# Optimization experiments

Hardware: AMD Instinct MI355X
Metric: run time of the kernel (lower is better)

Reference implementation:

```python
import jax, jax.numpy as jnp
import numpy as np

B, T, D_IN, H, NUM_LAYERS = 64, 512, 512, 500, 2


def _lstm_dir(x, mask, W_ih, W_hh, b, reverse):
    """One unidirectional LSTM over padded batch. x:[B,T,D], mask:[B,T,1] bool.
    AllenNLP AugmentedLstm gate order: input, forget, memory(cell), output."""
    bsz = x.shape[0]
    h_dim = W_hh.shape[1]
    # Precompute all input-side gate projections in one big GEMM: [B,T,4H]
    x_gates = jnp.einsum('btd,gd->btg', x, W_ih) + b

    def step(carry, inp):
        h, c = carry
        gx, m = inp  # gx:[B,4H], m:[B,1]
        gates = gx + h @ W_hh.T
        i, f, g, o = jnp.split(gates, 4, axis=-1)
        i = jax.nn.sigmoid(i)
        f = jax.nn.sigmoid(f)
        g = jnp.tanh(g)
        o = jax.nn.sigmoid(o)
        c_new = f * c + i * g
        h_new = o * jnp.tanh(c_new)
        h = jnp.where(m, h_new, h)
        c = jnp.where(m, c_new, c)
        return (h, c), h * m  # padded positions emit zeros (like pad_packed_sequence)

    init = (jnp.zeros((bsz, h_dim), x.dtype), jnp.zeros((bsz, h_dim), x.dtype))
    xs = (jnp.swapaxes(x_gates, 0, 1), jnp.swapaxes(mask, 0, 1))
    _, ys = jax.lax.scan(step, init, xs, reverse=reverse)
    return jnp.swapaxes(ys, 0, 1)  # [B,T,H]


def _stacked_bilstm(seqs, mask, params):
    x = seqs
    for (Wf_ih, Wf_hh, bf, Wb_ih, Wb_hh, bb) in params:
        fwd = _lstm_dir(x, mask, Wf_ih, Wf_hh, bf, reverse=False)
        bwd = _lstm_dir(x, mask, Wb_ih, Wb_hh, bb, reverse=True)
        x = jnp.concatenate([fwd, bwd], axis=-1)
    return x


def setup_inputs() -> dict:
    key = jax.random.key(0)
    ks = jax.random.split(key, 16)
    seqs = jax.random.normal(ks[0], (B, T, D_IN), dtype=jnp.float32)
    lengths = jnp.clip(jax.random.randint(ks[1], (B,), 0, T + 1), 1, T).astype(jnp.int64)
    inp = {'seqs': seqs, 'lengths': lengths}
    scale = 0.05
    d_in = D_IN
    idx = 2
    for l in range(NUM_LAYERS):
        for d in ('f', 'b'):
            inp[f'W_ih{l}{d}'] = jax.random.normal(ks[idx], (4 * H, d_in), dtype=jnp.float32) * scale; idx += 1
            inp[f'W_hh{l}{d}'] = jax.random.normal(ks[idx], (4 * H, H), dtype=jnp.float32) * scale; idx += 1
            inp[f'b{l}{d}'] = jnp.zeros((4 * H,), dtype=jnp.float32)
        d_in = 2 * H
    return inp


def reference(seqs, lengths, W_ih0f, W_hh0f, b0f, W_ih0b, W_hh0b, b0b,
              W_ih1f, W_hh1f, b1f, W_ih1b, W_hh1b, b1b):
    mask = (jnp.arange(T)[None, :] < lengths[:, None])[..., None]  # [B,T,1] bool
    params = [
        (W_ih0f, W_hh0f, b0f, W_ih0b, W_hh0b, b0b),
        (W_ih1f, W_hh1f, b1f, W_ih1b, W_hh1b, b1b),
    ]
    return _stacked_bilstm(seqs, mask, params)  # [B,T,2H]
```

## Files before the change

kernel.cpp:

```cpp
#include <hip/hip_runtime.h>
#include <cstdint>
#include <cstddef>

#define BB   64
#define TT   512
#define HH   500
#define G4H  2000
#define KPAD 512
#define TCH  64
#define D1P  1024
#define NPAD 2048
#define UPB  16
#define NB2  32
#define WSL2 (32 * 64 * 512)

typedef _Float16 v8h __attribute__((ext_vector_type(8)));
typedef _Float16 v4h __attribute__((ext_vector_type(4)));
typedef float    v4f __attribute__((ext_vector_type(4)));

union F16x8 { unsigned long long u[2]; float4 f4; v8h h; };
union H16B  { _Float16 f; unsigned short u; };

__device__ __forceinline__ float sigm(float x) { return 1.f / (1.f + __expf(-x)); }
__device__ __forceinline__ float tanh_fast(float x) {
    float e = __expf(2.f * x);
    return 1.f - 2.f / (e + 1.f);
}

__device__ __forceinline__ void gload_lds16(const _Float16* src, _Float16* dst) {
    __builtin_amdgcn_global_load_lds(
        (const __attribute__((address_space(1))) void*)src,
        (__attribute__((address_space(3))) void*)dst, 16, 0, 0);
}


__global__ __launch_bounds__(256) void pad_whh16_kernel(
    const float* __restrict__ w0, const float* __restrict__ w1,
    const float* __restrict__ w2, const float* __restrict__ w3,
    _Float16* __restrict__ dst)
{
    int idx = blockIdx.x * 256 + threadIdx.x;
    int k = idx & 511;
    int t = idx >> 9;
    int r = t & 63;  t >>= 6;
    int bi = t & 31;
    int ld = t >> 5;
    int g = r >> 4, j = r & 15;
    int u = bi * UPB + j;
    const float* src = (ld == 0) ? w0 : (ld == 1) ? w1 : (ld == 2) ? w2 : w3;
    float val = (u < HH && k < HH) ? src[(size_t)(g * HH + u) * HH + k] : 0.f;
    dst[idx] = (_Float16)val;
}

__global__ __launch_bounds__(256) void pad_wih16_kernel(
    const float* __restrict__ wf, const float* __restrict__ wb,
    _Float16* __restrict__ dst, int ksrc, int kshift)
{
    int idx = blockIdx.x * 256 + threadIdx.x;
    int kdst = 1 << kshift;
    int k = idx & (kdst - 1);
    int n = (idx >> kshift) & (NPAD - 1);
    int d = idx >> (kshift + 11);
    int bi = n >> 6, r = n & 63, g = r >> 4, j = r & 15;
    int u = bi * UPB + j;
    const float* src = d ? wb : wf;
    float v = (u < HH && k < ksrc) ? src[(size_t)(g * HH + u) * ksrc + k] : 0.f;
    dst[idx] = (_Float16)v;
}

__global__ __launch_bounds__(256) void bias_perm_kernel(
    const float* __restrict__ b0f_, const float* __restrict__ b0b_,
    const float* __restrict__ b1f_, const float* __restrict__ b1b_,
    float* __restrict__ dst)
{
    int idx = blockIdx.x * 256 + threadIdx.x;
    int n = idx & (NPAD - 1);
    int ld = idx >> 11;
    int bi = n >> 6, r = n & 63, g = r >> 4, j = r & 15;
    int u = bi * UPB + j;
    const float* src = (ld == 0) ? b0f_ : (ld == 1) ? b0b_ : (ld == 2) ? b1f_ : b1b_;
    dst[idx] = (u < HH) ? src[g * HH + u] : 0.f;
}

__global__ __launch_bounds__(256) void f32to16x4_kernel(
    const float* __restrict__ src, _Float16* __restrict__ dst)
{
    int idx = blockIdx.x * 256 + threadIdx.x;
    float4 v = ((const float4*)src)[idx];
    v4h o;
    o[0] = (_Float16)v.x; o[1] = (_Float16)v.y;
    o[2] = (_Float16)v.z; o[3] = (_Float16)v.w;
    ((v4h*)dst)[idx] = o;
}

#define BM 128
#define BN 128
#define BKG 64

__device__ __forceinline__ void gemm_body(
    int g, _Float16* smemh,
    const _Float16* __restrict__ A16, int K,
    const _Float16* __restrict__ W16,
    const float* __restrict__ bf_, const float* __restrict__ bb_,
    float* __restrict__ gates, int t0f, int t0b)
{
    const int mtile = g & 31;
    const int ntile = (g >> 5) & 15;
    const int dir   = g >> 9;
    const int t0  = dir ? t0b : t0f;
    const _Float16* W = W16 + (size_t)dir * NPAD * K;
    const float* bias = dir ? bb_ : bf_;
    const int tid  = threadIdx.x;
    const int lane = tid & 63;
    const int wv = __builtin_amdgcn_readfirstlane(tid >> 6);
    const int wm = wv >> 1, wn = wv & 1;

    _Float16* Asm = smemh;
    _Float16* Bsm = smemh + BM * BKG;

    const _Float16* aPtr[4];
    const _Float16* bPtr[4];
    #pragma unroll
    for (int it = 0; it < 4; ++it) {
        const int s = tid + it * 256;
        const int row = s >> 3;
        const int kswz = ((s ^ row) & 7) << 3;
        const int rg = mtile * BM + row;
        const int b = rg >> 6;
        const int t = t0 + (rg & 63);
        aPtr[it] = A16 + (size_t)(b * TT + t) * K + kswz;
        bPtr[it] = W + (size_t)(ntile * BN + row) * K + kswz;
    }

    v4f acc[4][4];
    #pragma unroll
    for (int mt = 0; mt < 4; ++mt)
        #pragma unroll
        for (int nt = 0; nt < 4; ++nt) acc[mt][nt] = (v4f)(0.f);

    for (int k0 = 0; k0 < K; k0 += BKG) {
        #pragma unroll
        for (int it = 0; it < 4; ++it) {
            gload_lds16(aPtr[it] + k0, &Asm[(tid + it * 256) * 8]);
            gload_lds16(bPtr[it] + k0, &Bsm[(tid + it * 256) * 8]);
        }
        __syncthreads();
        #pragma unroll
        for (int kk = 0; kk < 2; ++kk) {
            v8h af[4], bw[4];
            #pragma unroll
            for (int mt = 0; mt < 4; ++mt) {
                const int row = wm * 64 + mt * 16 + (lane & 15);
                const int slot = (kk * 4 + (lane >> 4)) ^ (row & 7);
                af[mt] = *(const v8h*)&Asm[row * BKG + slot * 8];
            }
            #pragma unroll
            for (int nt = 0; nt < 4; ++nt) {
                const int row = wn * 64 + nt * 16 + (lane & 15);
                const int slot = (kk * 4 + (lane >> 4)) ^ (row & 7);
                bw[nt] = *(const v8h*)&Bsm[row * BKG + slot * 8];
            }
            #pragma unroll
            for (int mt = 0; mt < 4; ++mt)
                #pragma unroll
                for (int nt = 0; nt < 4; ++nt)
                    acc[mt][nt] = __builtin_amdgcn_mfma_f32_16x16x32_f16(
                        af[mt], bw[nt], acc[mt][nt], 0, 0, 0);
        }
        __syncthreads();
    }

    float* gout = gates + (size_t)dir * (BB * TCH * NPAD);
    const int colBase = ntile * BN + wn * 64 + (lane & 15);
    const int rowBase = mtile * BM + wm * 64 + ((lane >> 4) * 4);
    #pragma unroll
    for (int nt = 0; nt < 4; ++nt) {
        const int n = colBase + nt * 16;
        const float bv = bias[n];
        #pragma unroll
        for (int mt = 0; mt < 4; ++mt) {
            const int r = rowBase + mt * 16;
            const int b = r >> 6;
            const int tl = r & 63;
            float* gp = gout + (size_t)(b * TCH + tl) * NPAD + n;
            #pragma unroll
            for (int i = 0; i < 4; ++i)
                gp[(size_t)i * NPAD] = acc[mt][nt][i] + bv;
        }
    }
}

__global__ __launch_bounds__(256, 2) void gemm16_kernel(
    const _Float16* __restrict__ A16, int K,
    const _Float16* __restrict__ W16,
    const float* __restrict__ bf_, const float* __restrict__ bb_,
    float* __restrict__ gates, int t0f, int t0b)
{
    extern __shared__ _Float16 smemh[];
    gemm_body(blockIdx.x, smemh, A16, K, W16, bf_, bb_, gates, t0f, t0b);
}

__global__ __launch_bounds__(256, 1) void fused_phase_kernel(
    const float*    __restrict__ gates,
    const _Float16* __restrict__ whh16,
    const int*      __restrict__ lengths,
    _Float16* __restrict__ h16,
    float*    __restrict__ cbuf,
    void*     __restrict__ yout, int y_ld, int yF16,
    int s0, int gstep0,
    unsigned int* __restrict__ flags,
    const _Float16* __restrict__ A16, int K,
    const _Float16* __restrict__ W16,
    const float* __restrict__ bfp, const float* __restrict__ bbp,
    float* __restrict__ gatesN, int nt0f, int nt0b, int doGemm)
{
    extern __shared__ _Float16 smemh[];

    if (blockIdx.x >= 64) {
        if (doGemm)
            gemm_body(blockIdx.x - 64, smemh, A16, K, W16, bfp, bbp,
                      gatesN, nt0f, nt0b);
        return;
    }

    const int tid  = threadIdx.x;
    const int dir  = (blockIdx.x >= NB2) ? 1 : 0;
    const int bi   = blockIdx.x - dir * NB2;
    const int u0   = bi * UPB;
    const int lane = tid & 63;
    const int w    = __builtin_amdgcn_readfirstlane(tid >> 6);

    _Float16* Wl = smemh;

    {
        const _Float16* wsrc = whh16 + (size_t)dir * WSL2 + (size_t)bi * 64 * 512;
        #pragma unroll
        for (int it = 0; it < 16; ++it) {
            const int slot = tid + it * 256;
            const int r = slot >> 6, sp = slot & 63;
            gload_lds16(wsrc + (size_t)r * 512 + ((sp ^ (r & 7)) << 3),
                        Wl + slot * 8);
        }
    }

    const int jn = lane & 15;
    const int hi = lane >> 4;
    const bool uval = (u0 + jn) < HH;
    const int b0 = w * 16 + hi * 4;

    int lenv[4];
    float cst[4], hpv[4];
    #pragma unroll
    for (int i = 0; i < 4; ++i) {
        const int b = b0 + i;
        lenv[i] = lengths[b];
        cst[i]  = cbuf[(size_t)(dir * BB + b) * KPAD + u0 + jn];
        hpv[i]  = (float)h16[((size_t)(dir * 2 + 0) * BB + b) * 512 + u0 + jn];
    }

    __syncthreads();

    const float* gb = gates + (size_t)dir * (BB * TCH * NPAD) + bi * 64 + jn;

    for (int sl = 0; sl < TCH; ++sl) {
        const int s   = s0 + sl;
        const int par = s & 1;
        const int t   = dir ? (TT - 1 - s) : s;
        const int tl  = dir ? (TCH - 1 - sl) : sl;

        F16x8 av[16];
        {
            const char* hb = (const char*)(h16 + (size_t)(dir * 2 + par) * BB * 512);
            const size_t base = ((size_t)(w * 16 + jn) * 512 + hi * 8) * 2;
            #pragma unroll
            for (int kt = 0; kt < 16; ++kt) {
                const unsigned long long* p =
                    (const unsigned long long*)(hb + base + (size_t)kt * 64);
                av[kt].u[0] = __hip_atomic_load(p,     __ATOMIC_RELAXED, __HIP_MEMORY_SCOPE_AGENT);
                av[kt].u[1] = __hip_atomic_load(p + 1, __ATOMIC_RELAXED, __HIP_MEMORY_SCOPE_AGENT);
            }
        }

        float gx[4][4];
        #pragma unroll
        for (int i = 0; i < 4; ++i) {
            const float* gp = gb + ((size_t)((b0 + i) * TCH + tl)) * NPAD;
            #pragma unroll
            for (int g = 0; g < 4; ++g) gx[g][i] = gp[g * 16];
        }

        v4f acc[4];
        #pragma unroll
        for (int g = 0; g < 4; ++g) acc[g] = (v4f)(0.f);
        #pragma unroll
        for (int kt = 0; kt < 16; ++kt) {
            #pragma unroll
            for (int g = 0; g < 4; ++g) {
                const int r = g * 16 + jn;
                const int sphys = (kt * 4 + hi) ^ (jn & 7);
                F16x8 bf; bf.f4 = *(const float4*)&Wl[r * 512 + sphys * 8];
                acc[g] = __builtin_amdgcn_mfma_f32_16x16x32_f16(
                    av[kt].h, bf.h, acc[g], 0, 0, 0);
            }
        }

        float ysv[4];
        #pragma unroll
        for (int i = 0; i < 4; ++i) {
            const bool msk = (t < lenv[i]);
            const float p0 = acc[0][i] + gx[0][i];
            const float p1 = acc[1][i] + gx[1][i];
            const float p2 = acc[2][i] + gx[2][i];
            const float p3 = acc[3][i] + gx[3][i];
            const float ig = sigm(p0);
            const float fg = sigm(p1);
            const float gg = tanh_fast(p2);
            const float og = sigm(p3);
            const float cn = fg * cst[i] + ig * gg;
            const float hn = og * tanh_fast(cn);
            cst[i] = msk ? cn : cst[i];
            hpv[i] = msk ? hn : hpv[i];
            ysv[i] = msk ? hn : 0.f;
        }

        if (uval) {
            #pragma unroll
            for (int i = 0; i < 4; ++i) {
                const int b = b0 + i;
                const size_t yoff = ((size_t)b * TT + t) * y_ld + dir * HH + u0 + jn;
                if (yF16) ((_Float16*)yout)[yoff] = (_Float16)ysv[i];
                else      ((float*)yout)[yoff]    = ysv[i];
                H16B hb16; hb16.f = (_Float16)hpv[i];
                __hip_atomic_store(
                    (unsigned short*)h16 +
                        ((size_t)(dir * 2 + (par ^ 1)) * BB + b) * 512 + u0 + jn,
                    hb16.u, __ATOMIC_RELAXED, __HIP_MEMORY_SCOPE_AGENT);
            }
        }

        __syncthreads();

        const unsigned int tgt = (unsigned int)(gstep0 + sl + 1);
        if (tid == 0)
            __hip_atomic_store(&flags[(dir * NB2 + bi) * 16], tgt,
                               __ATOMIC_RELAXED, __HIP_MEMORY_SCOPE_AGENT);
        if (tid < 64) {
            const int fi = lane & 31;
            for (;;) {
                unsigned int v = __hip_atomic_load(&flags[(dir * NB2 + fi) * 16],
                                                   __ATOMIC_RELAXED, __HIP_MEMORY_SCOPE_AGENT);
                if (__all(v >= tgt)) break;
                __builtin_amdgcn_s_sleep(2);
            }
        }
        __syncthreads();
    }

    if (uval) {
        #pragma unroll
        for (int i = 0; i < 4; ++i)
            cbuf[(size_t)(dir * BB + b0 + i) * KPAD + u0 + jn] = cst[i];
    }
}

extern "C" void kernel_launch(void* const* d_in, const int* in_sizes, int n_in,
                              void* d_out, int out_size, void* d_ws, size_t ws_size,
                              hipStream_t stream)
{
    (void)in_sizes; (void)n_in; (void)out_size; (void)ws_size;

    const float* seqs    = (const float*)d_in[0];
    const int*   lengths = (const int*)  d_in[1];
    const float* W_ih0f  = (const float*)d_in[2];
    const float* W_hh0f  = (const float*)d_in[3];
    const float* b0f     = (const float*)d_in[4];
    const float* W_ih0b  = (const float*)d_in[5];
    const float* W_hh0b  = (const float*)d_in[6];
    const float* b0b     = (const float*)d_in[7];
    const float* W_ih1f  = (const float*)d_in[8];
    const float* W_hh1f  = (const float*)d_in[9];
    const float* b1f     = (const float*)d_in[10];
    const float* W_ih1b  = (const float*)d_in[11];
    const float* W_hh1b  = (const float*)d_in[12];
    const float* b1b     = (const float*)d_in[13];

    char* ws = (char*)d_ws;
    const size_t SZ_GATES = (size_t)2 * BB * TCH * NPAD * 4;
    const size_t SZ_SEQ16 = (size_t)BB * TT * 512 * 2;
    const size_t SZ_OUT16 = (size_t)BB * TT * D1P * 2;
    const size_t SZ_WIH0  = (size_t)2 * NPAD * 512 * 2;
    const size_t SZ_WIH1  = (size_t)2 * NPAD * D1P * 2;
    const size_t SZ_WHH16 = (size_t)4 * WSL2 * 2;
    const size_t SZ_BPERM = (size_t)4 * NPAD * 4;
    const size_t SZ_H16   = (size_t)2 * 2 * BB * 512 * 2;
    const size_t SZ_CBUF  = (size_t)2 * BB * KPAD * 4;
    const size_t SZ_FLAGS = (size_t)64 * 16 * 4;

    size_t off = 0;
    float*     gatesA = (float*)(ws + off);     off += SZ_GATES;
    float*     gatesB = (float*)(ws + off);     off += SZ_GATES;
    _Float16*  seq16  = (_Float16*)(ws + off);  off += SZ_SEQ16;
    _Float16*  out16  = (_Float16*)(ws + off);  off += SZ_OUT16;
    _Float16*  wih016 = (_Float16*)(ws + off);  off += SZ_WIH0;
    _Float16*  wih116 = (_Float16*)(ws + off);  off += SZ_WIH1;
    _Float16*  whh16  = (_Float16*)(ws + off);  off += SZ_WHH16;
    float*     bperm  = (float*)(ws + off);     off += SZ_BPERM;
    _Float16*  h16    = (_Float16*)(ws + off);  off += SZ_H16;
    float*     cbuf   = (float*)(ws + off);     off += SZ_CBUF;
    unsigned int* flags = (unsigned int*)(ws + off);  off += SZ_FLAGS;

    pad_whh16_kernel<<<16384, 256, 0, stream>>>(W_hh0f, W_hh0b, W_hh1f, W_hh1b, whh16);
    pad_wih16_kernel<<<8192,  256, 0, stream>>>(W_ih0f, W_ih0b, wih016, 512, 9);
    pad_wih16_kernel<<<16384, 256, 0, stream>>>(W_ih1f, W_ih1b, wih116, 1000, 10);
    bias_perm_kernel<<<32,    256, 0, stream>>>(b0f, b0b, b1f, b1b, bperm);
    f32to16x4_kernel<<<16384, 256, 0, stream>>>(seqs, seq16);
    hipMemsetAsync(out16, 0, SZ_OUT16, stream);
    hipMemsetAsync(flags, 0, SZ_FLAGS, stream);

    for (int layer = 0; layer < 2; ++layer) {
        hipMemsetAsync(h16, 0, SZ_H16, stream);
        hipMemsetAsync(cbuf, 0, SZ_CBUF, stream);

        const _Float16* A16  = layer ? out16 : seq16;
        const int       K    = layer ? D1P : 512;
        const _Float16* WL   = layer ? wih116 : wih016;
        const float*    bfp  = bperm + (size_t)(layer * 2 + 0) * NPAD;
        const float*    bbp  = bperm + (size_t)(layer * 2 + 1) * NPAD;
        const _Float16* whhL = whh16 + (size_t)layer * 2 * WSL2;
        void*           yo   = layer ? d_out : (void*)out16;
        const int       y_ld = layer ? 1000 : D1P;
        const int       yF16 = layer ? 0 : 1;

        gemm16_kernel<<<1024, 256, 32768, stream>>>(
            A16, K, WL, bfp, bbp, gatesA, 0, TT - TCH);

        for (int ph = 0; ph < 8; ++ph) {
            float* gcur = (ph & 1) ? gatesB : gatesA;
            float* gnxt = (ph & 1) ? gatesA : gatesB;
            const int doG  = (ph < 7) ? 1 : 0;
            const int nt0f = (ph + 1) * TCH;
            const int nt0b = TT - TCH * (ph + 2);
            const int gstep0 = layer * TT + ph * TCH;
            fused_phase_kernel<<<doG ? 1088 : 64, 256, 65536, stream>>>(
                gcur, whhL, lengths, h16, cbuf, yo, y_ld, yF16,
                ph * TCH, gstep0, flags,
                A16, K, WL, bfp, bbp, gnxt, nt0f, nt0b, doG);
        }
    }
}
```

Measured before the change: 6.621 ms.

## Prefetch next-step gate inputs during barrier spin and use static shared memory

The input-gate values for the next timestep are now loaded right after this block publishes its flag and before it spins on the barrier, so their global-load latency overlaps the cross-block wait. The first step's values are loaded before the loop. The h16 atomic stores are issued ahead of the y output stores so peers see new state sooner, and the spin sleep is shortened. Shared memory moves from dynamic to static allocation, with the fused kernel sized at 96KB instead of 64KB, which may change occupancy of the GEMM blocks launched alongside it.

```diff
diff --git a/kernel.cpp b/kernel.cpp
--- a/kernel.cpp
+++ b/kernel.cpp
@@ -196,8 +196,8 @@
     const float* __restrict__ bf_, const float* __restrict__ bb_,
     float* __restrict__ gates, int t0f, int t0b)
 {
-    extern __shared__ _Float16 smemh[];
-    gemm_body(blockIdx.x, smemh, A16, K, W16, bf_, bb_, gates, t0f, t0b);
+    __shared__ _Float16 smemg[BM * BKG + BN * BKG];
+    gemm_body(blockIdx.x, smemg, A16, K, W16, bf_, bb_, gates, t0f, t0b);
 }
 
 __global__ __launch_bounds__(256, 1) void fused_phase_kernel(
@@ -214,7 +214,7 @@
     const float* __restrict__ bfp, const float* __restrict__ bbp,
     float* __restrict__ gatesN, int nt0f, int nt0b, int doGemm)
 {
-    extern __shared__ _Float16 smemh[];
+    __shared__ _Float16 smemh[49152];
 
     if (blockIdx.x >= 64) {
         if (doGemm)
@@ -224,8 +224,8 @@
     }
 
     const int tid  = threadIdx.x;
-    const int dir  = (blockIdx.x >= NB2) ? 1 : 0;
-    const int bi   = blockIdx.x - dir * NB2;
+    const int dir  = blockIdx.x >> 5;
+    const int bi   = blockIdx.x & 31;
     const int u0   = bi * UPB;
     const int lane = tid & 63;
     const int w    = __builtin_amdgcn_readfirstlane(tid >> 6);
@@ -262,11 +262,21 @@
 
     const float* gb = gates + (size_t)dir * (BB * TCH * NPAD) + bi * 64 + jn;
 
+    float gxv[4][4];
+    {
+        const int tl0 = dir ? (TCH - 1) : 0;
+        #pragma unroll
+        for (int i = 0; i < 4; ++i) {
+            const float* gp = gb + ((size_t)((b0 + i) * TCH + tl0)) * NPAD;
+            #pragma unroll
+            for (int g = 0; g < 4; ++g) gxv[g][i] = gp[g * 16];
+        }
+    }
+
     for (int sl = 0; sl < TCH; ++sl) {
         const int s   = s0 + sl;
         const int par = s & 1;
         const int t   = dir ? (TT - 1 - s) : s;
-        const int tl  = dir ? (TCH - 1 - sl) : sl;
 
         F16x8 av[16];
         {
@@ -279,14 +289,6 @@
                 av[kt].u[0] = __hip_atomic_load(p,     __ATOMIC_RELAXED, __HIP_MEMORY_SCOPE_AGENT);
                 av[kt].u[1] = __hip_atomic_load(p + 1, __ATOMIC_RELAXED, __HIP_MEMORY_SCOPE_AGENT);
             }
-        }
-
-        float gx[4][4];
-        #pragma unroll
-        for (int i = 0; i < 4; ++i) {
-            const float* gp = gb + ((size_t)((b0 + i) * TCH + tl)) * NPAD;
-            #pragma unroll
-            for (int g = 0; g < 4; ++g) gx[g][i] = gp[g * 16];
         }
 
         v4f acc[4];
@@ -308,10 +310,10 @@
         #pragma unroll
         for (int i = 0; i < 4; ++i) {
             const bool msk = (t < lenv[i]);
-            const float p0 = acc[0][i] + gx[0][i];
-            const float p1 = acc[1][i] + gx[1][i];
-            const float p2 = acc[2][i] + gx[2][i];
-            const float p3 = acc[3][i] + gx[3][i];
+            const float p0 = acc[0][i] + gxv[0][i];
+            const float p1 = acc[1][i] + gxv[1][i];
+            const float p2 = acc[2][i] + gxv[2][i];
+            const float p3 = acc[3][i] + gxv[3][i];
             const float ig = sigm(p0);
             const float fg = sigm(p1);
             const float gg = tanh_fast(p2);
@@ -327,15 +329,19 @@
             #pragma unroll
             for (int i = 0; i < 4; ++i) {
                 const int b = b0 + i;
-                const size_t yoff = ((size_t)b * TT + t) * y_ld + dir * HH + u0 + jn;
-                if (yF16) ((_Float16*)yout)[yoff] = (_Float16)ysv[i];
-                else      ((float*)yout)[yoff]    = ysv[i];
                 H16B hb16; hb16.f = (_Float16)hpv[i];
                 __hip_atomic_store(
                     (unsigned short*)h16 +
                         ((size_t)(dir * 2 + (par ^ 1)) * BB + b) * 512 + u0 + jn,
                     hb16.u, __ATOMIC_RELAXED, __HIP_MEMORY_SCOPE_AGENT);
             }
+            #pragma unroll
+            for (int i = 0; i < 4; ++i) {
+                const int b = b0 + i;
+                const size_t yoff = ((size_t)b * TT + t) * y_ld + dir * HH + u0 + jn;
+                if (yF16) ((_Float16*)yout)[yoff] = (_Float16)ysv[i];
+                else      ((float*)yout)[yoff]    = ysv[i];
+            }
         }
 
         __syncthreads();
@@ -344,16 +350,38 @@
         if (tid == 0)
             __hip_atomic_store(&flags[(dir * NB2 + bi) * 16], tgt,
                                __ATOMIC_RELAXED, __HIP_MEMORY_SCOPE_AGENT);
+
+        float gxn[4][4];
+        const bool hasNext = (sl + 1 < TCH);
+        if (hasNext) {
+            const int tln = dir ? (TCH - 2 - sl) : (sl + 1);
+            #pragma unroll
+            for (int i = 0; i < 4; ++i) {
+                const float* gp = gb + ((size_t)((b0 + i) * TCH + tln)) * NPAD;
+                #pragma unroll
+                for (int g = 0; g < 4; ++g) gxn[g][i] = gp[g * 16];
+            }
+        }
+        asm volatile("" ::: "memory");
+
         if (tid < 64) {
             const int fi = lane & 31;
+            const unsigned int* fp = flags + (size_t)(dir * NB2 + fi) * 16;
             for (;;) {
-                unsigned int v = __hip_atomic_load(&flags[(dir * NB2 + fi) * 16],
-                                                   __ATOMIC_RELAXED, __HIP_MEMORY_SCOPE_AGENT);
+                unsigned int v = __hip_atomic_load(fp, __ATOMIC_RELAXED,
+                                                   __HIP_MEMORY_SCOPE_AGENT);
                 if (__all(v >= tgt)) break;
-                __builtin_amdgcn_s_sleep(2);
+                __builtin_amdgcn_s_sleep(1);
             }
         }
         __syncthreads();
+
+        if (hasNext) {
+            #pragma unroll
+            for (int g = 0; g < 4; ++g)
+                #pragma unroll
+                for (int i = 0; i < 4; ++i) gxv[g][i] = gxn[g][i];
+        }
     }
 
     if (uval) {
@@ -431,7 +459,7 @@
         const int       y_ld = layer ? 1000 : D1P;
         const int       yF16 = layer ? 0 : 1;
 
-        gemm16_kernel<<<1024, 256, 32768, stream>>>(
+        gemm16_kernel<<<1024, 256, 0, stream>>>(
             A16, K, WL, bfp, bbp, gatesA, 0, TT - TCH);
 
         for (int ph = 0; ph < 8; ++ph) {
@@ -441,7 +469,7 @@
             const int nt0f = (ph + 1) * TCH;
             const int nt0b = TT - TCH * (ph + 2);
             const int gstep0 = layer * TT + ph * TCH;
-            fused_phase_kernel<<<doG ? 1088 : 64, 256, 65536, stream>>>(
+            fused_phase_kernel<<<doG ? 1088 : 64, 256, 0, stream>>>(
                 gcur, whhL, lengths, h16, cbuf, yo, y_ld, yF16,
                 ph * TCH, gstep0, flags,
                 A16, K, WL, bfp, bbp, gnxt, nt0f, nt0b, doG);
```

After: 6.471 ms. -2.3%, faster.
